# Kernel optimization log

Hardware: AMD Instinct MI355X
Metric: run time of the kernel (lower is better)

Reference implementation:

```python
import jax, jax.numpy as jnp
import numpy as np

N, T, C1, C2, H = 32, 64, 128, 256, 512
LN2 = float(np.log(2.0))
EPS = 1e-8  # torch CosineSimilarity default eps


def setup_inputs() -> dict:
    key = jax.random.key(0)
    ks = jax.random.split(key, 16)
    g = lambda k, shape, fan: jax.random.normal(k, shape, jnp.float32) / np.sqrt(fan)
    inp = {
        "h0": jax.random.normal(ks[0], (N, H), jnp.float32),
        "c0": jax.random.normal(ks[1], (N, C1, C2), jnp.float32),
        "c_x": jax.random.normal(ks[2], (N, T, C1, C2), jnp.float32),
        # linear_k / linear_b / linear_e / linear_v (torch Linear: y = x W^T + b)
        "Wk": g(ks[3], (C2, H), H), "bk": jnp.zeros((C2,), jnp.float32),
        "Wb": g(ks[4], (1, H), H),  "bb": jnp.zeros((1,), jnp.float32),
        "We": g(ks[5], (C2, H), H), "be": jnp.zeros((C2,), jnp.float32),
        "Wv": g(ks[6], (C2, H), H), "bv": jnp.zeros((C2,), jnp.float32),
        # GRUCell(C2 -> H): packed [r|z|n] gates
        "W_ih": g(ks[7], (3 * H, C2), C2), "b_ih": jnp.zeros((3 * H,), jnp.float32),
        "W_hh": g(ks[8], (3 * H, H), H),   "b_hh": jnp.zeros((3 * H,), jnp.float32),
    }
    return inp


def _gru_cell(x, h, W_ih, b_ih, W_hh, b_hh):
    gi = x @ W_ih.T + b_ih  # (N, 3H)
    gh = h @ W_hh.T + b_hh
    i_r, i_z, i_n = jnp.split(gi, 3, axis=-1)
    h_r, h_z, h_n = jnp.split(gh, 3, axis=-1)
    r = jax.nn.sigmoid(i_r + h_r)
    z = jax.nn.sigmoid(i_z + h_z)
    n = jnp.tanh(i_n + r * h_n)
    return (1.0 - z) * n + z * h


def _ntm_step(p, h_prev, c_prev, cx):
    # h_prev: (N,H), c_prev/cx: (N,C1,C2)
    k = h_prev @ p["Wk"].T + p["bk"]              # (N,C2) key
    beta_pre = h_prev @ p["Wb"].T + p["bb"]       # (N,1)
    bpos = jnp.maximum(beta_pre, 0.0)
    bneg = jnp.minimum(beta_pre, 0.0)
    beta = jnp.log1p(jnp.exp(bneg)) + bpos + jnp.log1p(jnp.exp(-bpos)) + (1.0 - LN2)
    # cosine similarity along C2 between each memory row and the key
    num = jnp.einsum("nic,nc->ni", cx, k)         # (N,C1)
    cn = jnp.linalg.norm(cx, axis=2)              # (N,C1)
    kn = jnp.linalg.norm(k, axis=1, keepdims=True)  # (N,1)
    s = num / jnp.maximum(cn * kn, EPS)
    w = jax.nn.softmax(s * beta, axis=1)          # (N,C1) addressing weights
    r = jnp.einsum("ni,nic->nc", w, cx)           # (N,C2) read vector
    h = _gru_cell(r, h_prev, p["W_ih"], p["b_ih"], p["W_hh"], p["b_hh"])
    e = jax.nn.sigmoid(h @ p["We"].T + p["be"])   # (N,C2) erase
    v = h @ p["Wv"].T + p["bv"]                   # (N,C2) add
    wc = w[:, :, None]                            # (N,C1,1)
    c_new = c_prev * (1.0 - wc * e[:, None, :]) + wc * v[:, None, :]
    return h, c_new


def _forward(h0, c0, c_x, Wk, bk, Wb, bb, We, be, Wv, bv, W_ih, b_ih, W_hh, b_hh):
    p = dict(Wk=Wk, bk=bk, Wb=Wb, bb=bb, We=We, be=be, Wv=Wv, bv=bv,
             W_ih=W_ih, b_ih=b_ih, W_hh=W_hh, b_hh=b_hh)

    def step(carry, cx_t):
        h, c = carry
        h2, c2 = _ntm_step(p, h, c, cx_t)
        return (h2, c2), (h2, c2)

    _, (hs, cs) = jax.lax.scan(step, (h0, c0), jnp.swapaxes(c_x, 0, 1))
    # (T,N,...) -> (N,T,...)
    return jnp.swapaxes(hs, 0, 1), jnp.swapaxes(cs, 0, 1)


def reference(h0, c0, c_x, Wk, bk, Wb, bb, We, be, Wv, bv, W_ih, b_ih, W_hh, b_hh):
    return _forward(h0, c0, c_x, Wk, bk, Wb, bb, We, be, Wv, bv, W_ih, b_ih, W_hh, b_hh)
```

## Files before the change

kernel.cpp:

```cpp
#include <hip/hip_runtime.h>
#include <math.h>


#define NBAT 32
#define TSTEPS 64
#define C1D 128
#define C2D 256
#define HD 512
#define NBLK 128
#define LN2F 0.6931471805599453f
#define PSTRIDE 296

typedef float f32x4 __attribute__((ext_vector_type(4)));

static __device__ __forceinline__ float dot4f(float4 a, float4 b) {
  return a.x * b.x + a.y * b.y + a.z * b.z + a.w * b.w;
}
static __device__ __forceinline__ float sigm(float x) { return 1.0f / (1.0f + __expf(-x)); }

static __device__ __forceinline__ float aload(const float* p) {
  return __hip_atomic_load(p, __ATOMIC_RELAXED, __HIP_MEMORY_SCOPE_AGENT);
}
static __device__ __forceinline__ void astore(float* p, float v) {
  __hip_atomic_store(p, v, __ATOMIC_RELAXED, __HIP_MEMORY_SCOPE_AGENT);
}
static __device__ __forceinline__ float2 aload2(const float* p) {
  unsigned long long u = __hip_atomic_load((const unsigned long long*)p,
                                           __ATOMIC_RELAXED, __HIP_MEMORY_SCOPE_AGENT);
  union { unsigned long long u; float2 f; } c;
  c.u = u;
  return c.f;
}
static __device__ __forceinline__ void astore2(float* p, float a, float b) {
  union { float f[2]; unsigned long long u; } c;
  c.f[0] = a; c.f[1] = b;
  __hip_atomic_store((unsigned long long*)p, c.u, __ATOMIC_RELAXED, __HIP_MEMORY_SCOPE_AGENT);
}
static __device__ __forceinline__ float4 aload4(const float* p) {
  const float2 lo = aload2(p), hi = aload2(p + 2);
  return make_float4(lo.x, lo.y, hi.x, hi.y);
}
static __device__ __forceinline__ unsigned aloadu(const unsigned* p) {
  return __hip_atomic_load(p, __ATOMIC_RELAXED, __HIP_MEMORY_SCOPE_AGENT);
}
static __device__ __forceinline__ void astoreu(unsigned* p, unsigned v) {
  __hip_atomic_store(p, v, __ATOMIC_RELAXED, __HIP_MEMORY_SCOPE_AGENT);
}
static __device__ __forceinline__ void spinu(const unsigned* p, unsigned tgt) {
  while (aloadu(p) < tgt) __builtin_amdgcn_s_sleep(4);
}

#define BLOCK_FENCE() \
  do { asm volatile("s_waitcnt vmcnt(0) lgkmcnt(0)" ::: "memory"); __syncthreads(); } while (0)

__global__ void __launch_bounds__(256) ntm_chain(
    const float* __restrict__ h0, const float* __restrict__ c_x,
    const float* __restrict__ Wk, const float* __restrict__ bk,
    const float* __restrict__ Wb, const float* __restrict__ bb,
    const float* __restrict__ We, const float* __restrict__ be,
    const float* __restrict__ Wv, const float* __restrict__ bv,
    const float* __restrict__ Wih, const float* __restrict__ bih,
    const float* __restrict__ Whh, const float* __restrict__ bhh,
    float* __restrict__ hs_out, float* __restrict__ wsf, unsigned* __restrict__ flags)
{
  const int tid = threadIdx.x;
  const int bid = blockIdx.x;
  const int lane = tid & 63;
  const int wid = tid >> 6;

  float* hb0   = wsf;
  float* hb1   = hb0 + NBAT * HD;
  float* kbuf  = hb1 + NBAT * HD;
  float* betab = kbuf + NBAT * C2D;
  float* rbuf  = betab + 64;
  float* part  = rbuf + NBAT * C2D;
  float* wbuf  = part + NBAT * 4 * PSTRIDE;
  float* earr  = wbuf + NBAT * TSTEPS * C1D;
  float* varr  = earr + NBAT * TSTEPS * C2D;

  __shared__ float s_tile[32 * C2D];
  __shared__ float s_r[NBAT * 264];
  __shared__ float s_wih[12 * 260];
  __shared__ float s_whh[12 * 516];
  __shared__ float s_wk[2 * 516];
  __shared__ float s_wev[8 * 516];
  __shared__ float s_wb[HD];
  __shared__ float s_k[C2D];
  __shared__ float s_sc[32];
  __shared__ float s_p[32];
  __shared__ float s_ml[8];
  __shared__ float s_misc[8];

  const int n_att = bid >> 2, q_att = bid & 3;
  const int j0 = bid * 4;
  const int kch = bid * 2;
  const int evch = (bid - 32) * 4;

  for (int idx = tid; idx < 12 * C2D; idx += 256) {
    const int row = idx >> 8, c = idx & (C2D - 1);
    const int f = row / 3, g = row % 3;
    s_wih[row * 260 + c] = Wih[(g * HD + j0 + f) * C2D + c];
  }
  for (int idx = tid; idx < 12 * HD; idx += 256) {
    const int row = idx >> 9, c = idx & (HD - 1);
    const int f = row / 3, g = row % 3;
    s_whh[row * 516 + c] = Whh[(g * HD + j0 + f) * HD + c];
  }
  for (int idx = tid; idx < 2 * HD; idx += 256) {
    const int row = idx >> 9, c = idx & (HD - 1);
    s_wk[row * 516 + c] = Wk[(kch + row) * HD + c];
  }
  if (bid >= 32 && bid < 96) {
    for (int idx = tid; idx < 8 * HD; idx += 256) {
      const int row = idx >> 9, c = idx & (HD - 1);
      const float* __restrict__ src = (row < 4) ? We : Wv;
      s_wev[row * 516 + c] = src[(evch + (row & 3)) * HD + c];
    }
  }
  for (int idx = tid; idx < HD; idx += 256) s_wb[idx] = Wb[idx];

  float4 pf[8];
  auto prefetch_issue = [&](int t) {
    const float* src = c_x + ((size_t)((n_att * TSTEPS + t) * C1D + q_att * 32)) * C2D + lane * 4;
#pragma unroll
    for (int k = 0; k < 8; ++k) pf[k] = *(const float4*)(src + (wid * 8 + k) * C2D);
  };
  auto prefetch_commit = [&]() {
#pragma unroll
    for (int k = 0; k < 8; ++k) *(float4*)(s_tile + (wid * 8 + k) * C2D + lane * 4) = pf[k];
  };

  auto proj_k = [&](const float* __restrict__ hsrc) {
    const int n = tid >> 3, s = tid & 7;
    const float* hp = hsrc + n * HD;
    float k0 = 0, k1 = 0, bp = 0;
#pragma unroll
    for (int x = 0; x < 16; ++x) {
      const int cix = s * 64 + ((4 * x + 8 * s) & 63);
      const float4 hv = aload4(hp + cix);
      k0 += dot4f(hv, *(const float4*)(s_wk + cix));
      k1 += dot4f(hv, *(const float4*)(s_wk + 516 + cix));
      if (bid == 0) bp += dot4f(hv, *(const float4*)(s_wb + cix));
    }
#pragma unroll
    for (int m = 1; m < 8; m <<= 1) { k0 += __shfl_xor(k0, m); k1 += __shfl_xor(k1, m); }
    if (bid == 0) {
#pragma unroll
      for (int m = 1; m < 8; m <<= 1) bp += __shfl_xor(bp, m);
    }
    if (s == 0) {
      astore2(kbuf + n * C2D + kch, k0 + bk[kch], k1 + bk[kch + 1]);
      if (bid == 0) {
        const float xb = bp + bb[0];
        const float bpos = fmaxf(xb, 0.f), bneg = fminf(xb, 0.f);
        astore(betab + n, log1pf(__expf(bneg)) + bpos + log1pf(__expf(-bpos)) + (1.0f - LN2F));
      }
    }
  };

  auto phase_ev = [&](const float* __restrict__ hsrc, int te) {
    const int n = tid >> 3, s = tid & 7;
    const float* hp = hsrc + n * HD;
    float e[4] = {0, 0, 0, 0}, v[4] = {0, 0, 0, 0};
#pragma unroll
    for (int x = 0; x < 16; ++x) {
      const int cix = s * 64 + ((4 * x + 8 * s) & 63);
      const float4 hv = aload4(hp + cix);
#pragma unroll
      for (int f = 0; f < 4; ++f) {
        e[f] += dot4f(hv, *(const float4*)(s_wev + f * 516 + cix));
        v[f] += dot4f(hv, *(const float4*)(s_wev + (4 + f) * 516 + cix));
      }
    }
#pragma unroll
    for (int m = 1; m < 8; m <<= 1) {
#pragma unroll
      for (int f = 0; f < 4; ++f) { e[f] += __shfl_xor(e[f], m); v[f] += __shfl_xor(v[f], m); }
    }
    if (s == 0) {
      *(float4*)(earr + (size_t)(n * TSTEPS + te) * C2D + evch) =
          make_float4(sigm(e[0] + be[evch]), sigm(e[1] + be[evch + 1]),
                      sigm(e[2] + be[evch + 2]), sigm(e[3] + be[evch + 3]));
      *(float4*)(varr + (size_t)(n * TSTEPS + te) * C2D + evch) =
          make_float4(v[0] + bv[evch], v[1] + bv[evch + 1],
                      v[2] + bv[evch + 2], v[3] + bv[evch + 3]);
    }
  };

  auto phase_attn = [&](int t) {
    if (tid < 64) {
      const float4 kv = aload4(kbuf + n_att * C2D + tid * 4);
      *(float4*)(s_k + tid * 4) = kv;
      float sq = kv.x * kv.x + kv.y * kv.y + kv.z * kv.z + kv.w * kv.w;
#pragma unroll
      for (int m = 1; m < 64; m <<= 1) sq += __shfl_xor(sq, m);
      if (tid == 0) s_misc[0] = sqrtf(sq);
    } else if (tid == 64) {
      s_misc[1] = aload(betab + n_att);
    }
    __syncthreads();
    {
      const int row = tid >> 3, s8 = tid & 7;
      const float* xp = s_tile + row * C2D + s8 * 32;
      const float* kp = s_k + s8 * 32;
      float np = 0, cp = 0;
#pragma unroll
      for (int x = 0; x < 8; ++x) {
        const float4 xv = *(const float4*)(xp + x * 4);
        np += dot4f(xv, *(const float4*)(kp + x * 4));
        cp += dot4f(xv, xv);
      }
      np += __shfl_xor(np, 1); cp += __shfl_xor(cp, 1);
      np += __shfl_xor(np, 2); cp += __shfl_xor(cp, 2);
      np += __shfl_xor(np, 4); cp += __shfl_xor(cp, 4);
      if (s8 == 0) s_sc[row] = s_misc[1] * np / fmaxf(sqrtf(cp) * s_misc[0], 1e-8f);
    }
    __syncthreads();
    float* pp = part + (size_t)(n_att * 4 + q_att) * PSTRIDE;
    if (tid < 32) {
      const float s = s_sc[tid];
      float mq = s;
#pragma unroll
      for (int m = 1; m < 32; m <<= 1) mq = fmaxf(mq, __shfl_xor(mq, m));
      const float p = __expf(s - mq);
      s_p[tid] = p;
      float lq = p;
#pragma unroll
      for (int m = 1; m < 32; m <<= 1) lq += __shfl_xor(lq, m);
      if (tid == 0) astore2(pp, mq, lq);
      astore(pp + 258 + tid, s);
    }
    __syncthreads();
    {
      const int c = tid;
      float acc = 0.f;
#pragma unroll 8
      for (int i = 0; i < 32; ++i) acc += s_p[i] * s_tile[i * C2D + c];
      astore(pp + 2 + c, acc);
    }
    BLOCK_FENCE();
    if (tid == 0) astoreu(flags + (128 + bid) * 32, (unsigned)(t + 1));
  };

  auto phase_combine = [&](int t) {
    const int n = bid >> 2;
    if (tid < 3) spinu(flags + (128 + bid + 1 + tid) * 32, (unsigned)(t + 1));
    __syncthreads();
    if (tid < 4) {
      const float2 ml = aload2(part + (size_t)(n * 4 + tid) * PSTRIDE);
      s_ml[2 * tid] = ml.x; s_ml[2 * tid + 1] = ml.y;
    }
    __syncthreads();
    const float M = fmaxf(fmaxf(s_ml[0], s_ml[2]), fmaxf(s_ml[4], s_ml[6]));
    const float sc0 = __expf(s_ml[0] - M), sc1 = __expf(s_ml[2] - M);
    const float sc2 = __expf(s_ml[4] - M), sc3 = __expf(s_ml[6] - M);
    const float invL = 1.f / (s_ml[1] * sc0 + s_ml[3] * sc1 + s_ml[5] * sc2 + s_ml[7] * sc3);
    if (tid < 128) {
      const int q = tid >> 5, i = tid & 31;
      const float s = aload(part + (size_t)(n * 4 + q) * PSTRIDE + 258 + i);
      wbuf[((size_t)n * TSTEPS + t) * C1D + tid] = __expf(s - M) * invL;
    }
    {
      const int c = tid;
      const float r = (sc0 * aload(part + (size_t)(n * 4 + 0) * PSTRIDE + 2 + c) +
                       sc1 * aload(part + (size_t)(n * 4 + 1) * PSTRIDE + 2 + c) +
                       sc2 * aload(part + (size_t)(n * 4 + 2) * PSTRIDE + 2 + c) +
                       sc3 * aload(part + (size_t)(n * 4 + 3) * PSTRIDE + 2 + c)) * invL;
      astore(rbuf + n * C2D + c, r);
    }
    BLOCK_FENCE();
    if (tid == 0) astoreu(flags + (256 + n) * 32, (unsigned)(t + 1));
  };

  auto phase_gru = [&](const float* __restrict__ hsrc, float* __restrict__ hdst, int t) {
#pragma unroll
    for (int idx = tid; idx < 2048; idx += 256) {
      const int n2 = idx >> 6, c4 = (idx & 63) * 4;
      const float4 rv = aload4(rbuf + n2 * C2D + c4);
      *(float4*)(s_r + n2 * 264 + c4) = rv;
    }
    __syncthreads();
    const int n = tid >> 3, s = tid & 7;
    float aR[4] = {0, 0, 0, 0}, aZ[4] = {0, 0, 0, 0};
    float aNi[4] = {0, 0, 0, 0}, aNh[4] = {0, 0, 0, 0};
    const float* rb = s_r + n * 264 + s * 32;
#pragma unroll
    for (int x = 0; x < 8; ++x) {
      const int o = (4 * x + 4 * s) & 31;
      const float4 rv = *(const float4*)(rb + o);
      const int cix = s * 32 + o;
#pragma unroll
      for (int f = 0; f < 4; ++f) {
        aR[f]  += dot4f(rv, *(const float4*)(s_wih + (f * 3 + 0) * 260 + cix));
        aZ[f]  += dot4f(rv, *(const float4*)(s_wih + (f * 3 + 1) * 260 + cix));
        aNi[f] += dot4f(rv, *(const float4*)(s_wih + (f * 3 + 2) * 260 + cix));
      }
    }
    const float* hb = hsrc + n * HD;
#pragma unroll
    for (int x = 0; x < 16; ++x) {
      const int cix = s * 64 + ((4 * x + 8 * s) & 63);
      const float4 hv = aload4(hb + cix);
#pragma unroll
      for (int f = 0; f < 4; ++f) {
        aR[f]  += dot4f(hv, *(const float4*)(s_whh + (f * 3 + 0) * 516 + cix));
        aZ[f]  += dot4f(hv, *(const float4*)(s_whh + (f * 3 + 1) * 516 + cix));
        aNh[f] += dot4f(hv, *(const float4*)(s_whh + (f * 3 + 2) * 516 + cix));
      }
    }
#pragma unroll
    for (int m = 1; m < 8; m <<= 1) {
#pragma unroll
      for (int f = 0; f < 4; ++f) {
        aR[f] += __shfl_xor(aR[f], m);
        aZ[f] += __shfl_xor(aZ[f], m);
        aNi[f] += __shfl_xor(aNi[f], m);
        aNh[f] += __shfl_xor(aNh[f], m);
      }
    }
    if (s == 0) {
      const float4 hp4 = aload4(hsrc + n * HD + j0);
      const float hpv[4] = {hp4.x, hp4.y, hp4.z, hp4.w};
      float hn[4];
#pragma unroll
      for (int f = 0; f < 4; ++f) {
        const int j = j0 + f;
        const float rg = sigm(aR[f] + bih[j] + bhh[j]);
        const float z = sigm(aZ[f] + bih[HD + j] + bhh[HD + j]);
        const float ng = tanhf(aNi[f] + bih[2 * HD + j] + rg * (aNh[f] + bhh[2 * HD + j]));
        hn[f] = (1.f - z) * ng + z * hpv[f];
      }
      astore2(hdst + n * HD + j0, hn[0], hn[1]);
      astore2(hdst + n * HD + j0 + 2, hn[2], hn[3]);
      *(float4*)(hs_out + (size_t)(n * TSTEPS + t) * HD + j0) =
          make_float4(hn[0], hn[1], hn[2], hn[3]);
    }
    BLOCK_FENCE();
    if (tid == 0) astoreu(flags + (288 + bid) * 32, (unsigned)(t + 1));
  };

  if (tid < 64) {
    const int base = bid * 128 + tid * 2;
    astore2(hb1 + base, h0[base], h0[base + 1]);
  }
  prefetch_issue(0);
  __syncthreads();
  prefetch_commit();
  proj_k(h0);
  BLOCK_FENCE();
  if (tid == 0) astoreu(flags + bid * 32, 1u);

  for (int t = 0; t < TSTEPS; ++t) {
    const float* hsrc = (t & 1) ? hb0 : hb1;
    float* hdst = (t & 1) ? hb1 : hb0;
    if (tid < 64) {
      spinu(flags + (2 * tid) * 32, (unsigned)(t + 1));
      spinu(flags + (2 * tid + 1) * 32, (unsigned)(t + 1));
    }
    __syncthreads();
    phase_attn(t);
    if (t < TSTEPS - 1) prefetch_issue(t + 1);
    if ((bid & 3) == 0) phase_combine(t);
    if (t < TSTEPS - 1) prefetch_commit();
    if (tid < 32) spinu(flags + (256 + tid) * 32, (unsigned)(t + 1));
    __syncthreads();
    phase_gru(hsrc, hdst, t);
    if (tid < 64) {
      spinu(flags + (288 + 2 * tid) * 32, (unsigned)(t + 1));
      spinu(flags + (288 + 2 * tid + 1) * 32, (unsigned)(t + 1));
    }
    __syncthreads();
    if (t < TSTEPS - 1) {
      proj_k(hdst);
      BLOCK_FENCE();
      if (tid == 0) astoreu(flags + bid * 32, (unsigned)(t + 2));
    }
    if (bid >= 32 && bid < 96) phase_ev(hdst, t);
  }
}

__global__ void __launch_bounds__(256) ntm_cscan(
    const float* __restrict__ c0, const float* __restrict__ wsf,
    float* __restrict__ out)
{
  const float* wbuf = wsf + 2 * NBAT * HD + NBAT * C2D + 64 + NBAT * C2D + NBAT * 4 * PSTRIDE;
  const float* earr = wbuf + NBAT * TSTEPS * C1D;
  const float* varr = earr + NBAT * TSTEPS * C2D;
  float* cs_out = out + NBAT * TSTEPS * HD;

  const int tid = threadIdx.x;
  const int lane = tid & 63, wid = tid >> 6;
  const int n = blockIdx.x >> 3, g = blockIdx.x & 7;
  const int i0 = g * 16 + wid * 4;

  f32x4 c[4];
#pragma unroll
  for (int r = 0; r < 4; ++r)
    c[r] = *(const f32x4*)(c0 + ((size_t)(n * C1D + i0 + r)) * C2D + lane * 4);

  const float* ep = earr + (size_t)n * TSTEPS * C2D + lane * 4;
  const float* vp = varr + (size_t)n * TSTEPS * C2D + lane * 4;
  const float* wp = wbuf + (size_t)n * TSTEPS * C1D + i0;

  f32x4 e_nxt = *(const f32x4*)(ep);
  f32x4 v_nxt = *(const f32x4*)(vp);
  for (int t = 0; t < TSTEPS; ++t) {
    const f32x4 e4 = e_nxt, v4 = v_nxt;
    if (t + 1 < TSTEPS) {
      e_nxt = *(const f32x4*)(ep + (t + 1) * C2D);
      v_nxt = *(const f32x4*)(vp + (t + 1) * C2D);
    }
#pragma unroll
    for (int r = 0; r < 4; ++r) {
      const float wr = wp[t * C1D + r];
      c[r] = c[r] * (1.f - wr * e4) + wr * v4;
      __builtin_nontemporal_store(
          c[r], (f32x4*)(cs_out + ((size_t)((n * TSTEPS + t) * C1D + i0 + r)) * C2D + lane * 4));
    }
  }
}

extern "C" void kernel_launch(void* const* d_in, const int* in_sizes, int n_in,
                              void* d_out, int out_size, void* d_ws, size_t ws_size,
                              hipStream_t stream) {
  const float* h0 = (const float*)d_in[0];
  const float* c0 = (const float*)d_in[1];
  const float* c_x = (const float*)d_in[2];
  const float* Wk = (const float*)d_in[3];
  const float* bk = (const float*)d_in[4];
  const float* Wb = (const float*)d_in[5];
  const float* bb = (const float*)d_in[6];
  const float* We = (const float*)d_in[7];
  const float* be = (const float*)d_in[8];
  const float* Wv = (const float*)d_in[9];
  const float* bv = (const float*)d_in[10];
  const float* Wih = (const float*)d_in[11];
  const float* bih = (const float*)d_in[12];
  const float* Whh = (const float*)d_in[13];
  const float* bhh = (const float*)d_in[14];

  unsigned* flags = (unsigned*)d_ws;
  float* wsf = (float*)((char*)d_ws + 65536);

  (void)hipMemsetAsync(d_ws, 0, 65536, stream);
  ntm_chain<<<dim3(NBLK), dim3(256), 0, stream>>>(h0, c_x, Wk, bk, Wb, bb, We, be, Wv, bv,
                                                  Wih, bih, Whh, bhh, (float*)d_out, wsf, flags);
  ntm_cscan<<<dim3(256), dim3(256), 0, stream>>>(c0, wsf, (float*)d_out);
}
```

Baseline: 2.791 ms.

## Replace per-block flag spins with hierarchical barriers and fold combine into GRU

New measurement: 2.684 ms. 1.04x faster.

```diff
diff --git a/kernel.cpp b/kernel.cpp
--- a/kernel.cpp
+++ b/kernel.cpp
@@ -45,9 +45,6 @@
 }
 static __device__ __forceinline__ void astoreu(unsigned* p, unsigned v) {
   __hip_atomic_store(p, v, __ATOMIC_RELAXED, __HIP_MEMORY_SCOPE_AGENT);
-}
-static __device__ __forceinline__ void spinu(const unsigned* p, unsigned tgt) {
-  while (aloadu(p) < tgt) __builtin_amdgcn_s_sleep(4);
 }
 
 #define BLOCK_FENCE() \
@@ -68,12 +65,21 @@
   const int lane = tid & 63;
   const int wid = tid >> 6;
 
+  unsigned* A_int = flags + 0 * 32;
+  unsigned* A_fin = flags + 8 * 32;
+  unsigned* A_rel = flags + 16 * 32;
+  unsigned* H_int = flags + 32 * 32;
+  unsigned* H_fin = flags + 40 * 32;
+  unsigned* H_rel = flags + 48 * 32;
+  unsigned* P_int = flags + 64 * 32;
+  unsigned* P_fin = flags + 72 * 32;
+  unsigned* P_rel = flags + 80 * 32;
+
   float* hb0   = wsf;
   float* hb1   = hb0 + NBAT * HD;
   float* kbuf  = hb1 + NBAT * HD;
   float* betab = kbuf + NBAT * C2D;
-  float* rbuf  = betab + 64;
-  float* part  = rbuf + NBAT * C2D;
+  float* part  = betab + 64;
   float* wbuf  = part + NBAT * 4 * PSTRIDE;
   float* earr  = wbuf + NBAT * TSTEPS * C1D;
   float* varr  = earr + NBAT * TSTEPS * C2D;
@@ -83,18 +89,18 @@
   __shared__ float s_wih[12 * 260];
   __shared__ float s_whh[12 * 516];
   __shared__ float s_wk[2 * 516];
-  __shared__ float s_wev[8 * 516];
+  __shared__ float s_wev[4 * 516];
   __shared__ float s_wb[HD];
   __shared__ float s_k[C2D];
   __shared__ float s_sc[32];
   __shared__ float s_p[32];
-  __shared__ float s_ml[8];
+  __shared__ float s_scale[192];
   __shared__ float s_misc[8];
 
   const int n_att = bid >> 2, q_att = bid & 3;
   const int j0 = bid * 4;
   const int kch = bid * 2;
-  const int evch = (bid - 32) * 4;
+  const int evch = bid * 2;
 
   for (int idx = tid; idx < 12 * C2D; idx += 256) {
     const int row = idx >> 8, c = idx & (C2D - 1);
@@ -110,14 +116,34 @@
     const int row = idx >> 9, c = idx & (HD - 1);
     s_wk[row * 516 + c] = Wk[(kch + row) * HD + c];
   }
-  if (bid >= 32 && bid < 96) {
-    for (int idx = tid; idx < 8 * HD; idx += 256) {
-      const int row = idx >> 9, c = idx & (HD - 1);
-      const float* __restrict__ src = (row < 4) ? We : Wv;
-      s_wev[row * 516 + c] = src[(evch + (row & 3)) * HD + c];
-    }
+  for (int idx = tid; idx < 4 * HD; idx += 256) {
+    const int row = idx >> 9, c = idx & (HD - 1);
+    const float* __restrict__ src = (row < 2) ? We : Wv;
+    s_wev[row * 516 + c] = src[(evch + (row & 1)) * HD + c];
   }
   for (int idx = tid; idx < HD; idx += 256) s_wb[idx] = Wb[idx];
+
+  auto arrive = [&](unsigned* intr, unsigned* fin, unsigned* rel, unsigned g) {
+    if (tid == 0) {
+      const unsigned old = __hip_atomic_fetch_add(intr + (bid >> 4) * 32, 1u,
+                                                  __ATOMIC_RELAXED, __HIP_MEMORY_SCOPE_AGENT);
+      if (old == 16u * g - 1u) {
+        const unsigned o2 = __hip_atomic_fetch_add(fin, 1u, __ATOMIC_RELAXED,
+                                                   __HIP_MEMORY_SCOPE_AGENT);
+        if (o2 == 8u * g - 1u) {
+#pragma unroll
+          for (int i = 0; i < 16; ++i) astoreu(rel + i * 32, g);
+        }
+      }
+    }
+  };
+  auto wait_rel = [&](unsigned* rel, unsigned g) {
+    if (tid == 0) {
+      const unsigned* p = rel + (bid & 15) * 32;
+      while (aloadu(p) < g) __builtin_amdgcn_s_sleep(2);
+    }
+    __syncthreads();
+  };
 
   float4 pf[8];
   auto prefetch_issue = [&](int t) {
@@ -161,29 +187,26 @@
   auto phase_ev = [&](const float* __restrict__ hsrc, int te) {
     const int n = tid >> 3, s = tid & 7;
     const float* hp = hsrc + n * HD;
-    float e[4] = {0, 0, 0, 0}, v[4] = {0, 0, 0, 0};
+    float e0 = 0, e1 = 0, v0 = 0, v1 = 0;
 #pragma unroll
     for (int x = 0; x < 16; ++x) {
       const int cix = s * 64 + ((4 * x + 8 * s) & 63);
       const float4 hv = aload4(hp + cix);
-#pragma unroll
-      for (int f = 0; f < 4; ++f) {
-        e[f] += dot4f(hv, *(const float4*)(s_wev + f * 516 + cix));
-        v[f] += dot4f(hv, *(const float4*)(s_wev + (4 + f) * 516 + cix));
-      }
+      e0 += dot4f(hv, *(const float4*)(s_wev + cix));
+      e1 += dot4f(hv, *(const float4*)(s_wev + 516 + cix));
+      v0 += dot4f(hv, *(const float4*)(s_wev + 1032 + cix));
+      v1 += dot4f(hv, *(const float4*)(s_wev + 1548 + cix));
     }
 #pragma unroll
     for (int m = 1; m < 8; m <<= 1) {
-#pragma unroll
-      for (int f = 0; f < 4; ++f) { e[f] += __shfl_xor(e[f], m); v[f] += __shfl_xor(v[f], m); }
+      e0 += __shfl_xor(e0, m); e1 += __shfl_xor(e1, m);
+      v0 += __shfl_xor(v0, m); v1 += __shfl_xor(v1, m);
     }
     if (s == 0) {
-      *(float4*)(earr + (size_t)(n * TSTEPS + te) * C2D + evch) =
-          make_float4(sigm(e[0] + be[evch]), sigm(e[1] + be[evch + 1]),
-                      sigm(e[2] + be[evch + 2]), sigm(e[3] + be[evch + 3]));
-      *(float4*)(varr + (size_t)(n * TSTEPS + te) * C2D + evch) =
-          make_float4(v[0] + bv[evch], v[1] + bv[evch + 1],
-                      v[2] + bv[evch + 2], v[3] + bv[evch + 3]);
+      *(float2*)(earr + (size_t)(n * TSTEPS + te) * C2D + evch) =
+          make_float2(sigm(e0 + be[evch]), sigm(e1 + be[evch + 1]));
+      *(float2*)(varr + (size_t)(n * TSTEPS + te) * C2D + evch) =
+          make_float2(v0 + bv[evch], v1 + bv[evch + 1]);
     }
   };
 
@@ -238,46 +261,47 @@
       for (int i = 0; i < 32; ++i) acc += s_p[i] * s_tile[i * C2D + c];
       astore(pp + 2 + c, acc);
     }
-    BLOCK_FENCE();
-    if (tid == 0) astoreu(flags + (128 + bid) * 32, (unsigned)(t + 1));
-  };
-
-  auto phase_combine = [&](int t) {
-    const int n = bid >> 2;
-    if (tid < 3) spinu(flags + (128 + bid + 1 + tid) * 32, (unsigned)(t + 1));
-    __syncthreads();
-    if (tid < 4) {
-      const float2 ml = aload2(part + (size_t)(n * 4 + tid) * PSTRIDE);
-      s_ml[2 * tid] = ml.x; s_ml[2 * tid + 1] = ml.y;
-    }
-    __syncthreads();
-    const float M = fmaxf(fmaxf(s_ml[0], s_ml[2]), fmaxf(s_ml[4], s_ml[6]));
-    const float sc0 = __expf(s_ml[0] - M), sc1 = __expf(s_ml[2] - M);
-    const float sc2 = __expf(s_ml[4] - M), sc3 = __expf(s_ml[6] - M);
-    const float invL = 1.f / (s_ml[1] * sc0 + s_ml[3] * sc1 + s_ml[5] * sc2 + s_ml[7] * sc3);
-    if (tid < 128) {
-      const int q = tid >> 5, i = tid & 31;
-      const float s = aload(part + (size_t)(n * 4 + q) * PSTRIDE + 258 + i);
-      wbuf[((size_t)n * TSTEPS + t) * C1D + tid] = __expf(s - M) * invL;
-    }
-    {
-      const int c = tid;
-      const float r = (sc0 * aload(part + (size_t)(n * 4 + 0) * PSTRIDE + 2 + c) +
-                       sc1 * aload(part + (size_t)(n * 4 + 1) * PSTRIDE + 2 + c) +
-                       sc2 * aload(part + (size_t)(n * 4 + 2) * PSTRIDE + 2 + c) +
-                       sc3 * aload(part + (size_t)(n * 4 + 3) * PSTRIDE + 2 + c)) * invL;
-      astore(rbuf + n * C2D + c, r);
-    }
-    BLOCK_FENCE();
-    if (tid == 0) astoreu(flags + (256 + n) * 32, (unsigned)(t + 1));
   };
 
   auto phase_gru = [&](const float* __restrict__ hsrc, float* __restrict__ hdst, int t) {
-#pragma unroll
+    if (tid < NBAT) {
+      const int n = tid;
+      float mq[4], lq[4];
+#pragma unroll
+      for (int q = 0; q < 4; ++q) {
+        const float2 ml = aload2(part + (size_t)(n * 4 + q) * PSTRIDE);
+        mq[q] = ml.x; lq[q] = ml.y;
+      }
+      const float M = fmaxf(fmaxf(mq[0], mq[1]), fmaxf(mq[2], mq[3]));
+      float x[4], L = 0.f;
+#pragma unroll
+      for (int q = 0; q < 4; ++q) { x[q] = __expf(mq[q] - M); L += lq[q] * x[q]; }
+      const float invL = 1.f / L;
+#pragma unroll
+      for (int q = 0; q < 4; ++q) s_scale[n * 4 + q] = x[q] * invL;
+      s_scale[128 + n] = M;
+      s_scale[160 + n] = invL;
+    }
+    __syncthreads();
     for (int idx = tid; idx < 2048; idx += 256) {
       const int n2 = idx >> 6, c4 = (idx & 63) * 4;
-      const float4 rv = aload4(rbuf + n2 * C2D + c4);
-      *(float4*)(s_r + n2 * 264 + c4) = rv;
+      const float4 r0 = aload4(part + (size_t)(n2 * 4 + 0) * PSTRIDE + 2 + c4);
+      const float4 r1 = aload4(part + (size_t)(n2 * 4 + 1) * PSTRIDE + 2 + c4);
+      const float4 r2 = aload4(part + (size_t)(n2 * 4 + 2) * PSTRIDE + 2 + c4);
+      const float4 r3 = aload4(part + (size_t)(n2 * 4 + 3) * PSTRIDE + 2 + c4);
+      const float a0 = s_scale[n2 * 4], a1 = s_scale[n2 * 4 + 1];
+      const float a2 = s_scale[n2 * 4 + 2], a3 = s_scale[n2 * 4 + 3];
+      *(float4*)(s_r + n2 * 264 + c4) = make_float4(
+          a0 * r0.x + a1 * r1.x + a2 * r2.x + a3 * r3.x,
+          a0 * r0.y + a1 * r1.y + a2 * r2.y + a3 * r3.y,
+          a0 * r0.z + a1 * r1.z + a2 * r2.z + a3 * r3.z,
+          a0 * r0.w + a1 * r1.w + a2 * r2.w + a3 * r3.w);
+    }
+    if (bid < NBAT && tid < 128) {
+      const int q = tid >> 5, i = tid & 31;
+      const float s = aload(part + (size_t)(bid * 4 + q) * PSTRIDE + 258 + i);
+      wbuf[((size_t)bid * TSTEPS + t) * C1D + tid] =
+          __expf(s - s_scale[128 + bid]) * s_scale[160 + bid];
     }
     __syncthreads();
     const int n = tid >> 3, s = tid & 7;
@@ -335,8 +359,6 @@
       *(float4*)(hs_out + (size_t)(n * TSTEPS + t) * HD + j0) =
           make_float4(hn[0], hn[1], hn[2], hn[3]);
     }
-    BLOCK_FENCE();
-    if (tid == 0) astoreu(flags + (288 + bid) * 32, (unsigned)(t + 1));
   };
 
   if (tid < 64) {
@@ -348,42 +370,39 @@
   prefetch_commit();
   proj_k(h0);
   BLOCK_FENCE();
-  if (tid == 0) astoreu(flags + bid * 32, 1u);
+  arrive(P_int, P_fin, P_rel, 1u);
 
   for (int t = 0; t < TSTEPS; ++t) {
+    const unsigned g = (unsigned)(t + 1);
     const float* hsrc = (t & 1) ? hb0 : hb1;
     float* hdst = (t & 1) ? hb1 : hb0;
-    if (tid < 64) {
-      spinu(flags + (2 * tid) * 32, (unsigned)(t + 1));
-      spinu(flags + (2 * tid + 1) * 32, (unsigned)(t + 1));
-    }
-    __syncthreads();
+
+    wait_rel(P_rel, g);
     phase_attn(t);
+    BLOCK_FENCE();
+    arrive(A_int, A_fin, A_rel, g);
+    if (t > 0) phase_ev(hsrc, t - 1);
     if (t < TSTEPS - 1) prefetch_issue(t + 1);
-    if ((bid & 3) == 0) phase_combine(t);
+    wait_rel(A_rel, g);
     if (t < TSTEPS - 1) prefetch_commit();
-    if (tid < 32) spinu(flags + (256 + tid) * 32, (unsigned)(t + 1));
-    __syncthreads();
     phase_gru(hsrc, hdst, t);
-    if (tid < 64) {
-      spinu(flags + (288 + 2 * tid) * 32, (unsigned)(t + 1));
-      spinu(flags + (288 + 2 * tid + 1) * 32, (unsigned)(t + 1));
-    }
-    __syncthreads();
+    BLOCK_FENCE();
+    arrive(H_int, H_fin, H_rel, g);
+    wait_rel(H_rel, g);
     if (t < TSTEPS - 1) {
       proj_k(hdst);
       BLOCK_FENCE();
-      if (tid == 0) astoreu(flags + bid * 32, (unsigned)(t + 2));
-    }
-    if (bid >= 32 && bid < 96) phase_ev(hdst, t);
-  }
+      arrive(P_int, P_fin, P_rel, g + 1u);
+    }
+  }
+  phase_ev(hb1, TSTEPS - 1);
 }
 
 __global__ void __launch_bounds__(256) ntm_cscan(
     const float* __restrict__ c0, const float* __restrict__ wsf,
     float* __restrict__ out)
 {
-  const float* wbuf = wsf + 2 * NBAT * HD + NBAT * C2D + 64 + NBAT * C2D + NBAT * 4 * PSTRIDE;
+  const float* wbuf = wsf + 2 * NBAT * HD + NBAT * C2D + 64 + NBAT * 4 * PSTRIDE;
   const float* earr = wbuf + NBAT * TSTEPS * C1D;
   const float* varr = earr + NBAT * TSTEPS * C2D;
   float* cs_out = out + NBAT * TSTEPS * HD;
@@ -440,9 +459,9 @@
   const float* bhh = (const float*)d_in[14];
 
   unsigned* flags = (unsigned*)d_ws;
-  float* wsf = (float*)((char*)d_ws + 65536);
-
-  (void)hipMemsetAsync(d_ws, 0, 65536, stream);
+  float* wsf = (float*)((char*)d_ws + 16384);
+
+  (void)hipMemsetAsync(d_ws, 0, 16384, stream);
   ntm_chain<<<dim3(NBLK), dim3(256), 0, stream>>>(h0, c_x, Wk, bk, Wb, bb, We, be, Wv, bv,
                                                   Wih, bih, Whh, bhh, (float*)d_out, wsf, flags);
   ntm_cscan<<<dim3(256), dim3(256), 0, stream>>>(c0, wsf, (float*)d_out);
```
